# Kernel tuning notes

Measured on AMD Instinct MI355X. Metric: run time of the kernel, lower is better.

The kernel has to match this reference:

```python
import jax, jax.numpy as jnp
import numpy as np

ALPHA = 2000.0   # alpha (bandwidth penalty)
K = 8            # number of modes
MAX_N = 20       # max ADMM iterations; tol=0 -> loop always runs MAX_N-1 iters
DC = False


def setup_inputs() -> dict:
    key = jax.random.key(0)
    signal = jax.random.normal(key, (16, 8192), dtype=jnp.float32)  # (C, T)
    return {"signal": signal}


def _forward(signal):
    C, T = signal.shape
    F = 2 * T
    # mirror extension -> (C, 2T)
    f = jnp.concatenate([signal[:, :T // 2][:, ::-1], signal, signal[:, T // 2:][:, ::-1]], axis=1)
    t = jnp.linspace(1.0 / F, 1.0, F)
    freqs = (t - 0.5 - 1.0 / F).astype(jnp.float32)                  # (F,)
    # NOTE: torch.fft.fftshift with default dim shifts ALL dims (incl. channel dim);
    # jnp.fft.fftshift with axes=None matches this behavior exactly.
    f_hat = jnp.fft.fftshift(jnp.fft.fft(f))
    f_hat_plus = f_hat.at[:, :F // 2].set(0)                         # zero negative freqs
    fpos = f_hat_plus.T.astype(jnp.complex64)                        # (F, C)
    freqs_c = freqs.astype(jnp.complex64)
    fh = freqs[F // 2:]                                              # positive freqs (F/2,)
    alpha_c = jnp.complex64(ALPHA)

    omega0 = ((0.5 / K) * jnp.arange(K, dtype=jnp.float32)).astype(jnp.complex64)  # init == 1
    u0 = jnp.zeros((F, K, C), jnp.complex64)
    sum0 = jnp.zeros((F, C), jnp.complex64)

    def omega_update(u_k):                                           # u_k: (F, C)
        p = jnp.abs(u_k[F // 2:, :]) ** 2                            # (F/2, C)
        return (jnp.sum(fh @ p) / jnp.sum(p)).astype(jnp.complex64)

    def step(carry, _):
        u_prev, omega_prev, sum_uk = carry
        sum_uk = sum_uk + u_prev[:, K - 1, :] - u_prev[:, 0, :]
        us, omegas = [], []
        for k in range(K):                                           # sequential mode recurrence
            if k > 0:
                sum_uk = sum_uk + us[k - 1] - u_prev[:, k, :]
            # torch uses omega from the PREVIOUS outer iteration for all modes
            denom = 1.0 + alpha_c * jnp.square(freqs_c - omega_prev[k])   # (F,)
            u_k = (fpos - sum_uk) / denom[:, None]   # lamda_hat stays 0 (never updated in torch)
            us.append(u_k)
            if k == 0 and DC:
                omegas.append(jnp.complex64(0.0))
            else:
                omegas.append(omega_update(u_k))
        u_curr = jnp.stack(us, axis=1)                               # (F, K, C)
        omega_curr = jnp.stack(omegas)                               # (K,)
        return (u_curr, omega_curr, sum_uk), omega_curr

    (u_fin, _, _), omega_hist = jax.lax.scan(step, (u0, omega0, sum0), None, length=MAX_N - 1)
    omega = jnp.concatenate([omega0[None, :], omega_hist], axis=0)   # (MAX_N, K)

    # Hermitian completion of the half-spectrum (matches torch index assignments & order)
    pos = u_fin[F // 2:, :, :]                                       # (F/2, K, C)
    u_hat = jnp.zeros((F, K, C), jnp.complex64)
    u_hat = u_hat.at[F // 2:].set(pos)
    u_hat = u_hat.at[jnp.arange(F // 2, 0, -1)].set(jnp.conj(pos))   # overwrites bin F/2 w/ conj
    u_hat = u_hat.at[0].set(jnp.conj(u_hat[-1]))

    u_time = jnp.fft.ifft(jnp.fft.ifftshift(u_hat, axes=0), axis=0).real  # (F, K, C)
    u_c = jnp.transpose(u_time, (1, 0, 2)).astype(jnp.complex64)          # (K, F, C)
    u_c = u_c[:, F // 4:3 * F // 4, :]                                    # crop mirror -> (K, T, C)
    u_hat2 = jnp.conj(jnp.fft.fftshift(jnp.fft.fft(u_c, axis=1), axes=1)) # (K, T, C)
    u_hat2 = jnp.transpose(u_hat2, (1, 0, 2))                             # (T, K, C)
    # torch applies ifftshift with dim=-1, which is the CHANNEL dim here; replicate faithfully
    u_out = jnp.fft.ifftshift(u_c, axes=-1).real                          # (K, T, C)
    return u_out, u_hat2, omega


def reference(signal):
    return _forward(signal)
```

## Files before the change

### kernel.cpp

```cpp
#include <hip/hip_runtime.h>
#include <math.h>

#define NPAIR 131072
#define STEPS 19
#define VMD_BLOCKS 256
#define ND_BANKS 16

#define SW(a) ((a) ^ (((a) >> 5) & 31))

#define LD_RLX(p)    __hip_atomic_load((p),       __ATOMIC_RELAXED, __HIP_MEMORY_SCOPE_AGENT)
#define ST_RLX(p,v)  __hip_atomic_store((p),(v),  __ATOMIC_RELAXED, __HIP_MEMORY_SCOPE_AGENT)
#define FAA_RLX(p,v) __hip_atomic_fetch_add((p),(v),__ATOMIC_RELAXED, __HIP_MEMORY_SCOPE_AGENT)

__device__ __forceinline__ float2 cadd(float2 a, float2 b){ return make_float2(a.x+b.x, a.y+b.y); }
__device__ __forceinline__ float2 csub(float2 a, float2 b){ return make_float2(a.x-b.x, a.y-b.y); }
__device__ __forceinline__ float2 cmul(float2 a, float2 b){
    return make_float2(a.x*b.x - a.y*b.y, a.x*b.y + a.y*b.x);
}
template<int SGN>
__device__ __forceinline__ float2 imul(float2 a){
    return (SGN > 0) ? make_float2(-a.y, a.x) : make_float2(a.y, -a.x);
}

template<int SGN>
__device__ __forceinline__ void dft8(const float2* a, float2* y){
    const float C = 0.70710678118654752f;
    const float sg = (SGN > 0) ? 1.f : -1.f;
    float2 t0 = cadd(a[0], a[4]), t1 = csub(a[0], a[4]);
    float2 t2 = cadd(a[2], a[6]), t3 = imul<SGN>(csub(a[2], a[6]));
    float2 E0 = cadd(t0, t2), E2 = csub(t0, t2), E1 = cadd(t1, t3), E3 = csub(t1, t3);
    float2 s0 = cadd(a[1], a[5]), s1 = csub(a[1], a[5]);
    float2 s2 = cadd(a[3], a[7]), s3 = imul<SGN>(csub(a[3], a[7]));
    float2 O0 = cadd(s0, s2), O2 = csub(s0, s2), O1 = cadd(s1, s3), O3 = csub(s1, s3);
    float2 w1 = make_float2(C, sg * C), w3 = make_float2(-C, sg * C);
    float2 R0 = O0, R1 = cmul(O1, w1), R2 = imul<SGN>(O2), R3 = cmul(O3, w3);
    y[0] = cadd(E0, R0); y[4] = csub(E0, R0);
    y[1] = cadd(E1, R1); y[5] = csub(E1, R1);
    y[2] = cadd(E2, R2); y[6] = csub(E2, R2);
    y[3] = cadd(E3, R3); y[7] = csub(E3, R3);
}

template<int SGN>
__device__ void lds_fft8192_r8(float2* lds, int tid){
    #pragma unroll
    for (int pi = 0; pi < 4; pi++){
        int ls = 3 * pi;
        int s  = 1 << ls;
        int nn = 8192 >> ls;
        int q = tid & (s - 1);
        float2 a[8], y[8];
        #pragma unroll
        for (int r = 0; r < 8; r++) a[r] = lds[SW(tid + (r << 10))];
        __syncthreads();
        dft8<SGN>(a, y);
        int p = tid >> ls;
        float ang = (float)(2 * p) / (float)nn;
        float sn, cs;
        sincospif(SGN > 0 ? ang : -ang, &sn, &cs);
        float2 w = make_float2(cs, sn);
        float2 wk = make_float2(1.f, 0.f);
        int o = q + ((tid - q) << 3);
        lds[SW(o)] = y[0];
        #pragma unroll
        for (int k = 1; k < 8; k++){
            wk = cmul(wk, w);
            lds[SW(o + (k << ls))] = cmul(y[k], wk);
        }
        __syncthreads();
    }
    #pragma unroll
    for (int w4 = 0; w4 < 4; w4++){
        int idx = (w4 << 10) + tid;
        float2 a = lds[SW(idx)], b = lds[SW(idx + 4096)];
        lds[SW(idx)]        = cadd(a, b);
        lds[SW(idx + 4096)] = csub(a, b);
    }
    __syncthreads();
}

__global__ __launch_bounds__(1024) void k_stageA(const float* __restrict__ sig,
                                                 float2* __restrict__ FPTA,
                                                 float2* __restrict__ FPTB,
                                                 double* __restrict__ D){
    extern __shared__ float2 lds[];
    int tid  = threadIdx.x;
    int bb   = blockIdx.x;
    for (int zi = bb * 1024 + tid; zi < 5400; zi += 32768)
        D[zi] = 0.0;
    int cw   = bb >> 1, half = bb & 1;
    int cs   = (cw + 8) & 15;
    const float* sp = sig + cs * 8192;
    #pragma unroll
    for (int r = 0; r < 8; r++){
        int p = r * 1024 + tid;
        int x = 2 * p + half;
        int mx = (x < 4096) ? (4095 - x) : ((x < 12288) ? (x - 4096) : (20479 - x));
        lds[SW(p)] = make_float2(sp[mx], 0.f);
    }
    __syncthreads();
    lds_fft8192_r8<-1>(lds, tid);
    float2* dst = (half == 0 ? FPTA : FPTB) + cw * 8192;
    #pragma unroll
    for (int r = 0; r < 8; r++){
        int j = r * 1024 + tid;
        dst[j] = lds[SW(j)];
    }
}

__global__ __launch_bounds__(512, 2) void k_vmd_all(const float2* __restrict__ FPTA,
                                                    const float2* __restrict__ FPTB,
                                                    float2* __restrict__ U,
                                                    double* __restrict__ D){
    double* NDB = D;
    int*    CNT = (int*)(D + 4864);

    int tid = blockIdx.x * 512 + threadIdx.x;
    int j = tid & 8191;
    double fr = (double)j / 16384.0;
    float2 Av = FPTA[tid], Bv = FPTB[tid];
    float snw, cnw;
    sincospif(-(float)j / 8192.0f, &snw, &cnw);
    float2 tw = cmul(Bv, make_float2(cnw, snw));
    float2 fv = make_float2(Av.x + tw.x, Av.y + tw.y);
    double fx = fv.x, fy = fv.y;
    float urx[8], ury[8];
    double om[8];
    #pragma unroll
    for (int k = 0; k < 8; k++){ urx[k] = 0.f; ury[k] = 0.f; om[k] = 0.0625 * (double)k; }
    __shared__ double lred[8][16];
    __shared__ double ndls[256];
    __shared__ double om_s[8];
    int lane = threadIdx.x & 63, wv = threadIdx.x >> 6;
    int mybank = (blockIdx.x & (ND_BANKS - 1)) * 16;
    int grp = blockIdx.x >> 4;

    for (int step = 0; step < STEPS; step++){
        if (step > 0){
            #pragma unroll
            for (int k = 0; k < 8; k++) om[k] = om_s[k];
        }
        double sx = 0.0, sy = 0.0;
        #pragma unroll
        for (int k = 1; k < 8; k++){ sx += (double)urx[k]; sy += (double)ury[k]; }
        double lx = 0.0, ly = 0.0, nloc[8], dloc[8];
        #pragma unroll
        for (int k = 0; k < 8; k++){
            if (k > 0){ sx += lx - (double)urx[k]; sy += ly - (double)ury[k]; }
            double d = fr - om[k];
            double den = 1.0 + 2000.0 * d * d;
            double nx = (fx - sx) / den, ny = (fy - sy) / den;
            urx[k] = (float)nx; ury[k] = (float)ny;
            lx = nx; ly = ny;
            double pw = nx * nx + ny * ny;
            nloc[k] = fr * pw; dloc[k] = pw;
        }
        double s8[8];
        {
            bool hi = (lane & 32) != 0;
            #pragma unroll
            for (int k = 0; k < 8; k++){
                double t = hi ? nloc[k] : dloc[k];
                double r = __shfl_xor(t, 32);
                s8[k] = (hi ? dloc[k] : nloc[k]) + r;
            }
        }
        double s4v[4];
        {
            bool hi = (lane & 16) != 0;
            #pragma unroll
            for (int k = 0; k < 4; k++){
                double t = hi ? s8[k] : s8[k + 4];
                double r = __shfl_xor(t, 16);
                s4v[k] = (hi ? s8[k + 4] : s8[k]) + r;
            }
        }
        double s2v[2];
        {
            bool hi = (lane & 8) != 0;
            #pragma unroll
            for (int k = 0; k < 2; k++){
                double t = hi ? s4v[k] : s4v[k + 2];
                double r = __shfl_xor(t, 8);
                s2v[k] = (hi ? s4v[k + 2] : s4v[k]) + r;
            }
        }
        double sv;
        {
            bool hi = (lane & 4) != 0;
            double t = hi ? s2v[0] : s2v[1];
            double r = __shfl_xor(t, 4);
            sv = (hi ? s2v[1] : s2v[0]) + r;
        }
        sv += __shfl_xor(sv, 2);
        sv += __shfl_xor(sv, 1);
        if ((lane & 3) == 0) lred[wv][lane >> 2] = sv;
        __syncthreads();
        if (threadIdx.x < 16){
            double sum = 0.0;
            #pragma unroll
            for (int w = 0; w < 8; w++) sum += lred[w][threadIdx.x];
            atomicAdd(&NDB[step * 256 + mybank + threadIdx.x], sum);
        }
        __syncthreads();
        if (step < STEPS - 1){
            if (threadIdx.x == 0){
                int target = 16 * (step + 1);
                int old = FAA_RLX(&CNT[grp * 32], 1);
                bool released = false;
                if (old == target - 1){
                    int rold = FAA_RLX(&CNT[512], 1);
                    if (rold == target - 1){
                        #pragma unroll
                        for (int g = 0; g < 16; g++)
                            ST_RLX(&CNT[576 + g * 32], step + 1);
                        released = true;
                    }
                }
                if (!released)
                    while (LD_RLX(&CNT[576 + grp * 32]) <= step)
                        __builtin_amdgcn_s_sleep(1);
            }
            __syncthreads();
            if (threadIdx.x < 256)
                ndls[threadIdx.x] = LD_RLX(&NDB[step * 256 + threadIdx.x]);
            __syncthreads();
            if (threadIdx.x < 8){
                double n_ = 0.0, d_ = 0.0;
                #pragma unroll
                for (int bk = 0; bk < ND_BANKS; bk++){
                    n_ += ndls[bk * 16 + threadIdx.x];
                    d_ += ndls[bk * 16 + 8 + threadIdx.x];
                }
                om_s[threadIdx.x] = n_ / d_;
            }
            __syncthreads();
        }
    }
    #pragma unroll
    for (int k = 0; k < 8; k++) U[k * NPAIR + tid] = make_float2(urx[k], ury[k]);
}

__global__ __launch_bounds__(1024) void k_stageCD(float2* __restrict__ U){
    extern __shared__ float2 lds[];
    int tid = threadIdx.x;
    int b = blockIdx.x;
    const float2* pos = U + b * 8192;
    float* slice = (float*)(U) + (size_t)b * 16384;
    const float inv = 1.0f / 16384.0f;
    #pragma unroll
    for (int r = 0; r < 8; r++){
        int p = r * 1024 + tid;
        float2 Hk, HkM;
        if (p == 0){
            Hk  = make_float2(pos[0].x, 0.f);
            HkM = make_float2(pos[8191].x, 0.f);
        } else {
            Hk = pos[p];
            float2 q2 = pos[8192 - p];
            HkM = make_float2(q2.x, -q2.y);
        }
        float2 S  = cadd(Hk, HkM);
        float2 Dv = csub(Hk, HkM);
        float sn, cn;
        sincospif((float)p / 8192.0f, &sn, &cn);
        float2 c = cmul(make_float2(cn, sn), Dv);
        lds[SW(p)] = make_float2(S.x - c.y, S.y + c.x);
    }
    __syncthreads();
    lds_fft8192_r8<1>(lds, tid);
    float2 zreg[4];
    #pragma unroll
    for (int q = 2; q < 6; q++){
        int n = q * 1024 + tid;
        float2 z = lds[SW(n)];
        zreg[q - 2] = make_float2(z.x * inv, z.y * inv);
        *(float2*)&slice[2 * n - 4096] = zreg[q - 2];
    }
    __syncthreads();
    #pragma unroll
    for (int q = 0; q < 4; q++){
        int n = (q + 2) * 1024 + tid;
        int t = 2 * n - 4096;
        lds[SW(t)]     = make_float2(zreg[q].x, 0.f);
        lds[SW(t + 1)] = make_float2(zreg[q].y, 0.f);
    }
    __syncthreads();
    lds_fft8192_r8<-1>(lds, tid);
    #pragma unroll
    for (int q = 0; q < 8; q++){
        int t = q * 1024 + tid;
        float2 Y = lds[SW(((q + 4) & 7) * 1024 + tid)];
        slice[8192 + t] = Y.x;
    }
}

__global__ __launch_bounds__(256) void k_outs(const float* __restrict__ U32,
                                              const double* __restrict__ ndb,
                                              float* __restrict__ out){
    __shared__ float smem[128 * 65];
    int bx = blockIdx.x;
    int tid = threadIdx.x;
    if (bx < 256){
        float (*tile)[257] = (float(*)[257])smem;
        int k  = bx >> 5;
        int t0 = (bx & 31) * 256;
        #pragma unroll
        for (int cw = 0; cw < 16; cw++)
            tile[cw][tid] = U32[((size_t)(k * 16 + cw)) * 16384 + t0 + tid];
        __syncthreads();
        #pragma unroll
        for (int i = 0; i < 16; i++){
            int flat = i * 256 + tid;
            int dt = flat >> 4, ch = flat & 15;
            int cw = (ch + 8) & 15;
            out[(size_t)k * 131072 + t0 * 16 + flat] = tile[cw][dt];
        }
    } else if (bx < 384){
        float (*tile)[65] = (float(*)[65])smem;
        int t0 = (bx - 256) * 64;
        #pragma unroll
        for (int i = 0; i < 32; i++){
            int flat = i * 256 + tid;
            int b = flat >> 6, dt = flat & 63;
            tile[b][dt] = U32[(size_t)b * 16384 + 8192 + t0 + dt];
        }
        __syncthreads();
        #pragma unroll
        for (int i = 0; i < 32; i++){
            int flat = i * 256 + tid;
            int dt = flat >> 7, b = flat & 127;
            out[1048576 + (size_t)(t0 + dt) * 128 + b] = tile[b][dt];
        }
    } else {
        int t = tid;
        if (t >= 160) return;
        int row = t >> 3, k = t & 7;
        double v;
        if (row == 0){
            v = 0.0625 * (double)k;
        } else {
            const double* r = ndb + (row - 1) * 256;
            double n_ = 0.0, d_ = 0.0;
            #pragma unroll
            for (int bk = 0; bk < ND_BANKS; bk++){
                n_ += r[bk * 16 + k];
                d_ += r[bk * 16 + 8 + k];
            }
            v = n_ / d_;
        }
        out[2097152 + t] = (float)v;
    }
}

extern "C" void kernel_launch(void* const* d_in, const int* in_sizes, int n_in,
                              void* d_out, int out_size, void* d_ws, size_t ws_size,
                              hipStream_t stream){
    const float* sig = (const float*)d_in[0];
    float* out = (float*)d_out;
    char* p = (char*)d_ws;
    float2* U    = (float2*)p;
    float2* FPTA = (float2*)p;
    float2* FPTB = (float2*)(p + (size_t)1 * 1024 * 1024);
    double* D    = (double*)(p + (size_t)8 * 1024 * 1024);

    k_stageA<<<dim3(32), dim3(1024), 65536, stream>>>(sig, FPTA, FPTB, D);
    k_vmd_all<<<dim3(VMD_BLOCKS), dim3(512), 0, stream>>>(FPTA, FPTB, U, D);
    k_stageCD<<<dim3(128), dim3(1024), 65536, stream>>>(U);
    k_outs<<<dim3(385), dim3(256), 0, stream>>>((const float*)U, D, out);
}
```

Measured before the change: 174.0 us.

## Replace atomic-counter grid barrier with flag-based dissemination barrier

Replaces the two-level fetch-add counter barrier with per-block flag stores. A leader in each group of 16 polls its group's flags, then writes a release flag into every group's slot, and each block polls the 16 release flags for its group. This removes serialized atomic read-modify-writes on shared counters and the single global root counter, aiming to shorten the per-step grid synchronization latency. In exchange there is more polling traffic, and CNT must be initialized to match the new layout (indices 0..511).

```diff
diff --git a/kernel.cpp b/kernel.cpp
--- a/kernel.cpp
+++ b/kernel.cpp
@@ -10,7 +10,6 @@
 
 #define LD_RLX(p)    __hip_atomic_load((p),       __ATOMIC_RELAXED, __HIP_MEMORY_SCOPE_AGENT)
 #define ST_RLX(p,v)  __hip_atomic_store((p),(v),  __ATOMIC_RELAXED, __HIP_MEMORY_SCOPE_AGENT)
-#define FAA_RLX(p,v) __hip_atomic_fetch_add((p),(v),__ATOMIC_RELAXED, __HIP_MEMORY_SCOPE_AGENT)
 
 __device__ __forceinline__ float2 cadd(float2 a, float2 b){ return make_float2(a.x+b.x, a.y+b.y); }
 __device__ __forceinline__ float2 csub(float2 a, float2 b){ return make_float2(a.x-b.x, a.y-b.y); }
@@ -133,6 +132,7 @@
     int lane = threadIdx.x & 63, wv = threadIdx.x >> 6;
     int mybank = (blockIdx.x & (ND_BANKS - 1)) * 16;
     int grp = blockIdx.x >> 4;
+    int idx16 = blockIdx.x & 15;
 
     for (int step = 0; step < STEPS; step++){
         if (step > 0){
@@ -204,21 +204,29 @@
         __syncthreads();
         if (step < STEPS - 1){
             if (threadIdx.x == 0){
-                int target = 16 * (step + 1);
-                int old = FAA_RLX(&CNT[grp * 32], 1);
-                bool released = false;
-                if (old == target - 1){
-                    int rold = FAA_RLX(&CNT[512], 1);
-                    if (rold == target - 1){
+                int tgt = step + 1;
+                ST_RLX(&CNT[grp * 16 + idx16], tgt);
+                if (idx16 == 0){
+                    const int* a = &CNT[grp * 16];
+                    bool ok;
+                    do {
+                        ok = true;
                         #pragma unroll
-                        for (int g = 0; g < 16; g++)
-                            ST_RLX(&CNT[576 + g * 32], step + 1);
-                        released = true;
-                    }
+                        for (int i = 0; i < 16; i++) ok &= (LD_RLX(&a[i]) >= tgt);
+                        if (!ok) __builtin_amdgcn_s_sleep(1);
+                    } while (!ok);
+                    #pragma unroll
+                    for (int r = 0; r < 16; r++)
+                        ST_RLX(&CNT[256 + r * 16 + grp], tgt);
                 }
-                if (!released)
-                    while (LD_RLX(&CNT[576 + grp * 32]) <= step)
-                        __builtin_amdgcn_s_sleep(1);
+                const int* rp = &CNT[256 + grp * 16];
+                bool ok;
+                do {
+                    ok = true;
+                    #pragma unroll
+                    for (int g = 0; g < 16; g++) ok &= (LD_RLX(&rp[g]) >= tgt);
+                    if (!ok) __builtin_amdgcn_s_sleep(1);
+                } while (!ok);
             }
             __syncthreads();
             if (threadIdx.x < 256)
```

Measured after the change: 239.6 us. +37.7%, slower.
